# Kernel optimization log

Hardware: AMD Instinct MI355X
Metric: run time of the kernel (lower is better)

Reference implementation:

```python
import jax, jax.numpy as jnp
import numpy as np

B, C, W, H = 32, 256, 32, 32


def setup_inputs() -> dict:
    key = jax.random.key(0)
    ks = jax.random.split(key, 9)
    s = 1.0 / np.sqrt(C)
    return {
        "x": jax.random.normal(ks[0], (B, C, W, H), dtype=jnp.float32),
        "Wq": jax.random.normal(ks[1], (C, C), dtype=jnp.float32) * s,
        "bq": jax.random.normal(ks[2], (C,), dtype=jnp.float32) * 0.01,
        "Wk": jax.random.normal(ks[3], (C, C), dtype=jnp.float32) * s,
        "bk": jax.random.normal(ks[4], (C,), dtype=jnp.float32) * 0.01,
        "Wv": jax.random.normal(ks[5], (C, C), dtype=jnp.float32) * s,
        "bv": jax.random.normal(ks[6], (C,), dtype=jnp.float32) * 0.01,
        "rel_h": jax.random.normal(ks[7], (1, C, 1, H), dtype=jnp.float32),
        "rel_w": jax.random.normal(ks[8], (1, C, W, 1), dtype=jnp.float32),
    }


def reference(x, Wq, bq, Wk, bk, Wv, bv, rel_h, rel_w):
    b, c, w, h = x.shape
    n = w * h
    xf = x.reshape(b, c, n)  # [B, C, N]
    # 1x1 conv == channel-mixing matmul (out_ch 'o' from in_ch 'c')
    q = jnp.einsum('oc,bcn->bon', Wq, xf) + bq[None, :, None]
    k = jnp.einsum('oc,bcn->bon', Wk, xf) + bk[None, :, None]
    v = jnp.einsum('oc,bcn->bon', Wv, xf) + bv[None, :, None]
    # content-content: q^T k -> [B, N, N]
    content_content = jnp.einsum('bci,bcj->bij', q, k)
    # relative position bias: (rel_h + rel_w) broadcasts to [1, C, W, H]
    rel = (rel_h + rel_w).reshape(c, n)  # [C, N]
    content_position = jnp.einsum('cp,bcj->bpj', rel, q)  # [B, N, N]
    attention = jax.nn.softmax(content_content + content_position, axis=-1)
    # out[b,c,i] = sum_j v[b,c,j] * attention[b,i,j]
    out = jnp.einsum('bcj,bij->bci', v, attention)
    return out.reshape(b, c, w, h)
```

## Files before the change

kernel.cpp:

```cpp
#include <hip/hip_runtime.h>


#define NB 32
#define NC 256
#define NNN 1024

typedef _Float16 f16;
typedef __attribute__((ext_vector_type(8))) _Float16 half8;
typedef __attribute__((ext_vector_type(4))) float f32x4;
typedef __attribute__((ext_vector_type(4))) float float4v;

__device__ __forceinline__ f32x4 mfma16(half8 a, half8 b, f32x4 c) {
  return __builtin_amdgcn_mfma_f32_16x16x32_f16(a, b, c, 0, 0, 0);
}
__device__ __forceinline__ float sel4(float a0, float a1, float a2, float a3, int r) {
  return r == 0 ? a0 : (r == 1 ? a1 : (r == 2 ? a2 : a3));
}
__device__ __forceinline__ void gload16(const f16* g, f16* l) {
  __builtin_amdgcn_global_load_lds(
      (const __attribute__((address_space(1))) void*)g,
      (__attribute__((address_space(3))) void*)l, 16, 0, 0);
}

__global__ __launch_bounds__(256) void k_prep(
    const float* __restrict__ Wq, const float* __restrict__ Wk,
    const float* __restrict__ Wv, const float* __restrict__ relh,
    const float* __restrict__ relw, f16* __restrict__ Wh, f16* __restrict__ RT) {
  int bid = blockIdx.x, tid = threadIdx.x;
  if (bid < 192) {
    int base = (bid * 256 + tid) * 4;
    int w = base >> 16, j = base & 65535;
    const float* src = (w == 0) ? Wq : ((w == 1) ? Wk : Wv);
    float4v v = *(const float4v*)(src + j);
    f16 h[4] = {(f16)v.x, (f16)v.y, (f16)v.z, (f16)v.w};
    *(half8*)0;
    Wh[base + 0] = h[0]; Wh[base + 1] = h[1]; Wh[base + 2] = h[2]; Wh[base + 3] = h[3];
  } else {
    int n = bid - 192;
    int c = tid;
    RT[n * NC + c] = (f16)(relw[c * 32 + (n >> 5)] + relh[c * 32 + (n & 31)]);
  }
}

__global__ __launch_bounds__(256, 4) void k_proj(
    const float* __restrict__ x, const f16* __restrict__ Wh,
    const float* __restrict__ bq, const float* __restrict__ bk,
    const float* __restrict__ bv,
    f16* __restrict__ KQ, f16* __restrict__ V) {
  int b = blockIdx.x >> 4;
  int n0 = (blockIdx.x & 15) << 6;
  int tid = threadIdx.x;
  int wave = tid >> 6, lane = tid & 63;
  int lq = lane & 15, g = lane >> 4;
  int ow = wave << 6;

  __shared__ f16 XS[64][256];

  {
    const float* xb = x + (size_t)b * NC * NNN + n0;
    int cq = tid >> 2;
    int nn = (tid & 3) << 4;
    #pragma unroll
    for (int cc = 0; cc < 4; ++cc) {
      int c = cc * 64 + cq;
      const float* src = xb + (size_t)c * NNN + nn;
      float vals[16];
      *(float4v*)(vals + 0)  = *(const float4v*)(src + 0);
      *(float4v*)(vals + 4)  = *(const float4v*)(src + 4);
      *(float4v*)(vals + 8)  = *(const float4v*)(src + 8);
      *(float4v*)(vals + 12) = *(const float4v*)(src + 12);
      int s = c >> 3;
      #pragma unroll
      for (int u = 0; u < 16; ++u) {
        int n = nn + u;
        int p = (s & 0x10) | ((s ^ (n & 15)) & 0xF);
        XS[n][p * 8 + (c & 7)] = (f16)vals[u];
      }
    }
  }
  __syncthreads();

  #pragma unroll 1
  for (int which = 0; which < 2; ++which) {
    const f16* Wp = Wh + which * 65536;
    const float* bias = which ? bk : bq;
    int koff = which ? 0 : 256;
    f32x4 acc[4][4];
    #pragma unroll
    for (int f = 0; f < 4; ++f) {
      float bf = bias[ow + 16 * f + lq];
      #pragma unroll
      for (int m = 0; m < 4; ++m) acc[m][f] = (f32x4){bf, bf, bf, bf};
    }
    #pragma unroll
    for (int kk = 0; kk < 8; ++kk) {
      int cb = kk * 32 + 8 * g;
      int s = 4 * kk + g;
      int p = (s & 0x10) | ((s ^ lq) & 0xF);
      half8 xa[4], wb[4];
      #pragma unroll
      for (int m = 0; m < 4; ++m)
        xa[m] = *(const half8*)(&XS[16 * m + lq][p * 8]);
      #pragma unroll
      for (int f = 0; f < 4; ++f)
        wb[f] = *(const half8*)(Wp + (size_t)(ow + 16 * f + lq) * NC + cb);
      #pragma unroll
      for (int m = 0; m < 4; ++m)
        #pragma unroll
        for (int f = 0; f < 4; ++f)
          acc[m][f] = mfma16(xa[m], wb[f], acc[m][f]);
    }
    #pragma unroll
    for (int m = 0; m < 4; ++m)
      #pragma unroll
      for (int f = 0; f < 4; ++f)
        #pragma unroll
        for (int r = 0; r < 4; ++r)
          KQ[((size_t)b * NNN + n0 + 16 * m + 4 * g + r) * 512 + koff + ow + 16 * f + lq] =
              (f16)acc[m][f][r];
  }

  {
    const f16* Wp = Wh + 2 * 65536;
    f32x4 acc[4][4];
    #pragma unroll
    for (int m = 0; m < 4; ++m)
      #pragma unroll
      for (int r = 0; r < 4; ++r) {
        float bf = bv[ow + 16 * m + 4 * g + r];
        #pragma unroll
        for (int f = 0; f < 4; ++f) acc[m][f][r] = bf;
      }
    #pragma unroll
    for (int kk = 0; kk < 8; ++kk) {
      int cb = kk * 32 + 8 * g;
      int s = 4 * kk + g;
      int p = (s & 0x10) | ((s ^ lq) & 0xF);
      half8 va[4], xb2[4];
      #pragma unroll
      for (int m = 0; m < 4; ++m)
        va[m] = *(const half8*)(Wp + (size_t)(ow + 16 * m + lq) * NC + cb);
      #pragma unroll
      for (int f = 0; f < 4; ++f)
        xb2[f] = *(const half8*)(&XS[16 * f + lq][p * 8]);
      #pragma unroll
      for (int m = 0; m < 4; ++m)
        #pragma unroll
        for (int f = 0; f < 4; ++f)
          acc[m][f] = mfma16(va[m], xb2[f], acc[m][f]);
    }
    #pragma unroll
    for (int m = 0; m < 4; ++m)
      #pragma unroll
      for (int f = 0; f < 4; ++f)
        #pragma unroll
        for (int r = 0; r < 4; ++r)
          V[((size_t)b * NC + ow + 16 * m + 4 * g + r) * NNN + n0 + 16 * f + lq] =
              (f16)acc[m][f][r];
  }
}

__global__ __launch_bounds__(256, 2) void k_flash3(
    const f16* __restrict__ KQ, const f16* __restrict__ V,
    const f16* __restrict__ RT, float* __restrict__ out) {
  int bid = blockIdx.x;
  int swz = (bid & 7) * 64 + (bid >> 3);
  int b = swz >> 4;
  int i0 = (swz & 15) << 6;
  int tid = threadIdx.x;
  int wave = tid >> 6, lane = tid & 63;
  int lq = lane & 15, g = lane >> 4;
  int iw = i0 + 16 * wave;

  __shared__ f16 KQS[2][32][512];
  __shared__ f16 Plds[4][16][40];

  const f16* KQb = KQ + ((size_t)b << 19);
  const f16* Vb = V + ((size_t)b << 18);

  half8 QA[16];
  #pragma unroll
  for (int kk = 0; kk < 8; ++kk)
    QA[kk] = *(const half8*)(KQb + ((size_t)(iw + lq) << 9) + 256 + kk * 32 + 8 * g);
  #pragma unroll
  for (int kk = 0; kk < 8; ++kk)
    QA[8 + kk] = *(const half8*)(RT + (size_t)(iw + lq) * NC + kk * 32 + 8 * g);

  f32x4 acc[16];
  #pragma unroll
  for (int cf = 0; cf < 16; ++cf) acc[cf] = (f32x4){0.f, 0.f, 0.f, 0.f};
  float m[4] = {-1e30f, -1e30f, -1e30f, -1e30f};
  float lsum[4] = {0.f, 0.f, 0.f, 0.f};

#define STAGE(JT, BUF)                                                        \
  {                                                                           \
    _Pragma("unroll")                                                         \
    for (int rr = 0; rr < 8; ++rr) {                                          \
      int r_ = wave * 8 + rr;                                                 \
      int slot_ = (lane & 0x30) | ((lane ^ (r_ & 15)) & 0xF);                 \
      gload16(KQb + ((size_t)((JT) * 32 + r_) << 9) + slot_ * 8,              \
              &KQS[BUF][r_][0]);                                              \
    }                                                                         \
  }

  STAGE(0, 0);
  asm volatile("s_waitcnt vmcnt(0)" ::: "memory");
  __syncthreads();

  int cur = 0;
  #pragma unroll 1
  for (int jt = 0; jt < 32; ++jt) {
    int j0 = jt * 32;
    if (jt < 31) {
      if (cur) STAGE(jt + 1, 0) else STAGE(jt + 1, 1);
    }
    f32x4 S0 = (f32x4){0.f, 0.f, 0.f, 0.f};
    f32x4 S1 = (f32x4){0.f, 0.f, 0.f, 0.f};
    const f16* KQSc = &KQS[cur][0][0];
    __builtin_amdgcn_s_setprio(1);
    #pragma unroll
    for (int kk = 0; kk < 16; ++kk) {
      int s = 4 * kk + g;
      int p = (s & 0x30) | ((s ^ lq) & 0xF);
      S0 = mfma16(QA[kk], *(const half8*)(KQSc + lq * 512 + p * 8), S0);
      S1 = mfma16(QA[kk], *(const half8*)(KQSc + (16 + lq) * 512 + p * 8), S1);
    }
    __builtin_amdgcn_s_setprio(0);

    float t[4];
    #pragma unroll
    for (int r = 0; r < 4; ++r) {
      float tt = fmaxf(S0[r], S1[r]);
      tt = fmaxf(tt, __shfl_xor(tt, 1));
      tt = fmaxf(tt, __shfl_xor(tt, 2));
      tt = fmaxf(tt, __shfl_xor(tt, 4));
      tt = fmaxf(tt, __shfl_xor(tt, 8));
      t[r] = tt;
    }
    bool grow = (t[0] > m[0] + 8.f) | (t[1] > m[1] + 8.f) |
                (t[2] > m[2] + 8.f) | (t[3] > m[3] + 8.f);
    if (__builtin_amdgcn_ballot_w64(grow)) {
      float sc[4];
      #pragma unroll
      for (int r = 0; r < 4; ++r) {
        float mn = fmaxf(m[r], t[r]);
        sc[r] = __expf(m[r] - mn);
        m[r] = mn;
        lsum[r] *= sc[r];
      }
      int srcl = (lq >> 2) << 4;
      float s0 = __shfl(sc[0], srcl);
      float s1 = __shfl(sc[1], srcl);
      float s2 = __shfl(sc[2], srcl);
      float s3 = __shfl(sc[3], srcl);
      float sci = sel4(s0, s1, s2, s3, lq & 3);
      #pragma unroll
      for (int cf = 0; cf < 16; ++cf) {
        acc[cf][0] *= sci; acc[cf][1] *= sci; acc[cf][2] *= sci; acc[cf][3] *= sci;
      }
    }
    #pragma unroll
    for (int r = 0; r < 4; ++r) {
      float p0 = __expf(S0[r] - m[r]);
      float p1 = __expf(S1[r] - m[r]);
      S0[r] = p0; S1[r] = p1;
      lsum[r] += p0 + p1;
    }

    #pragma unroll
    for (int r = 0; r < 4; ++r) {
      Plds[wave][4 * g + r][lq] = (f16)S0[r];
      Plds[wave][4 * g + r][16 + lq] = (f16)S1[r];
    }
    asm volatile("s_waitcnt lgkmcnt(0)" ::: "memory");
    __builtin_amdgcn_sched_barrier(0);
    half8 pa = *(const half8*)(&Plds[wave][lq][8 * g]);

    __builtin_amdgcn_s_setprio(1);
    #pragma unroll
    for (int cf = 0; cf < 16; ++cf) {
      half8 vv = *(const half8*)(Vb + ((size_t)(16 * cf + lq) << 10) + j0 + 8 * g);
      acc[cf] = mfma16(vv, pa, acc[cf]);
    }
    __builtin_amdgcn_s_setprio(0);

    asm volatile("s_waitcnt vmcnt(0)" ::: "memory");
    __syncthreads();
    cur ^= 1;
  }
#undef STAGE

  #pragma unroll
  for (int r = 0; r < 4; ++r) {
    float l = lsum[r];
    l += __shfl_xor(l, 1);
    l += __shfl_xor(l, 2);
    l += __shfl_xor(l, 4);
    l += __shfl_xor(l, 8);
    lsum[r] = 1.f / l;
  }
  float li;
  {
    int srcl = (lq >> 2) << 4;
    float l0 = __shfl(lsum[0], srcl);
    float l1 = __shfl(lsum[1], srcl);
    float l2 = __shfl(lsum[2], srcl);
    float l3 = __shfl(lsum[3], srcl);
    li = sel4(l0, l1, l2, l3, lq & 3);
  }
  #pragma unroll
  for (int cf = 0; cf < 16; ++cf)
    #pragma unroll
    for (int r = 0; r < 4; ++r)
      out[((size_t)(b * NC + 16 * cf + 4 * g + r) << 10) + iw + lq] = acc[cf][r] * li;
}

extern "C" void kernel_launch(void* const* d_in, const int* in_sizes, int n_in,
                              void* d_out, int out_size, void* d_ws, size_t ws_size,
                              hipStream_t stream) {
  const float* x = (const float*)d_in[0];
  const float* Wq = (const float*)d_in[1];
  const float* bq = (const float*)d_in[2];
  const float* Wk = (const float*)d_in[3];
  const float* bk = (const float*)d_in[4];
  const float* Wv = (const float*)d_in[5];
  const float* bv = (const float*)d_in[6];
  const float* relh = (const float*)d_in[7];
  const float* relw = (const float*)d_in[8];

  char* ws = (char*)d_ws;
  const size_t MB = 1 << 20;
  f16* KQ = (f16*)(ws);
  f16* V = (f16*)(ws + 32 * MB);
  f16* RT = (f16*)(ws + 48 * MB);
  f16* Wh = (f16*)(ws + 48 * MB + 512 * 1024);

  k_prep<<<dim3(1216), dim3(256), 0, stream>>>(Wq, Wk, Wv, relh, relw, Wh, RT);
  k_proj<<<dim3(512), dim3(256), 0, stream>>>(x, Wh, bq, bk, bv, KQ, V);
  k_flash3<<<dim3(512), dim3(256), 0, stream>>>(KQ, V, RT, (float*)d_out);
}
```

Baseline: 326.4 us.

## Add transpose pre-pass and restructure flash attention with 16-row triple buffering

Adds a separate kernel that converts x to fp16 and transposes it to a token-major layout, so the projection kernel can fill shared memory with direct global-to-LDS loads instead of scattered per-element writes. The attention kernel now processes 16 key rows per step with operands swapped, so each lane holds one query row. That removes the LDS round-trip for P and shrinks the row-max and row-sum reductions. It uses a three-buffer LDS pipeline with a partial vmcnt wait, and the smaller LDS footprint allows raising occupancy to 3 blocks. The trade-off is an extra launch and an extra pass over x through memory, plus the cost of holding half of P in registers across iterations.

```diff
diff --git a/kernel.cpp b/kernel.cpp
--- a/kernel.cpp
+++ b/kernel.cpp
@@ -6,15 +6,13 @@
 #define NNN 1024
 
 typedef _Float16 f16;
+typedef __attribute__((ext_vector_type(4))) _Float16 half4;
 typedef __attribute__((ext_vector_type(8))) _Float16 half8;
 typedef __attribute__((ext_vector_type(4))) float f32x4;
 typedef __attribute__((ext_vector_type(4))) float float4v;
 
 __device__ __forceinline__ f32x4 mfma16(half8 a, half8 b, f32x4 c) {
   return __builtin_amdgcn_mfma_f32_16x16x32_f16(a, b, c, 0, 0, 0);
-}
-__device__ __forceinline__ float sel4(float a0, float a1, float a2, float a3, int r) {
-  return r == 0 ? a0 : (r == 1 ? a1 : (r == 2 ? a2 : a3));
 }
 __device__ __forceinline__ void gload16(const f16* g, f16* l) {
   __builtin_amdgcn_global_load_lds(
@@ -32,9 +30,8 @@
     int w = base >> 16, j = base & 65535;
     const float* src = (w == 0) ? Wq : ((w == 1) ? Wk : Wv);
     float4v v = *(const float4v*)(src + j);
-    f16 h[4] = {(f16)v.x, (f16)v.y, (f16)v.z, (f16)v.w};
-    *(half8*)0;
-    Wh[base + 0] = h[0]; Wh[base + 1] = h[1]; Wh[base + 2] = h[2]; Wh[base + 3] = h[3];
+    Wh[base + 0] = (f16)v.x; Wh[base + 1] = (f16)v.y;
+    Wh[base + 2] = (f16)v.z; Wh[base + 3] = (f16)v.w;
   } else {
     int n = bid - 192;
     int c = tid;
@@ -42,8 +39,42 @@
   }
 }
 
+__global__ __launch_bounds__(256) void k_xpose(
+    const float* __restrict__ x, f16* __restrict__ xT) {
+  int bid = blockIdx.x;
+  int nt = bid & 15, ct = (bid >> 4) & 3, b = bid >> 6;
+  int c0 = ct << 6, n0 = nt << 6;
+  __shared__ f16 T[64][72];
+  int t = threadIdx.x;
+  {
+    int cl = t >> 2, n4 = (t & 3) << 4;
+    const float* src = x + ((size_t)(b * NC + c0 + cl) << 10) + n0 + n4;
+    float4v v0 = *(const float4v*)(src + 0);
+    float4v v1 = *(const float4v*)(src + 4);
+    float4v v2 = *(const float4v*)(src + 8);
+    float4v v3 = *(const float4v*)(src + 12);
+    f16* d = &T[cl][n4];
+    d[0]=(f16)v0.x; d[1]=(f16)v0.y; d[2]=(f16)v0.z; d[3]=(f16)v0.w;
+    d[4]=(f16)v1.x; d[5]=(f16)v1.y; d[6]=(f16)v1.z; d[7]=(f16)v1.w;
+    d[8]=(f16)v2.x; d[9]=(f16)v2.y; d[10]=(f16)v2.z; d[11]=(f16)v2.w;
+    d[12]=(f16)v3.x; d[13]=(f16)v3.y; d[14]=(f16)v3.z; d[15]=(f16)v3.w;
+  }
+  __syncthreads();
+  {
+    int nl = t >> 2, c16 = (t & 3) << 4;
+    half8 h0, h1;
+    #pragma unroll
+    for (int u = 0; u < 8; ++u) h0[u] = T[c16 + u][nl];
+    #pragma unroll
+    for (int u = 0; u < 8; ++u) h1[u] = T[c16 + 8 + u][nl];
+    f16* dst = xT + ((size_t)(b * NNN + n0 + nl) << 8) + c0 + c16;
+    *(half8*)(dst) = h0;
+    *(half8*)(dst + 8) = h1;
+  }
+}
+
 __global__ __launch_bounds__(256, 4) void k_proj(
-    const float* __restrict__ x, const f16* __restrict__ Wh,
+    const f16* __restrict__ xT, const f16* __restrict__ Wh,
     const float* __restrict__ bq, const float* __restrict__ bk,
     const float* __restrict__ bv,
     f16* __restrict__ KQ, f16* __restrict__ V) {
@@ -53,31 +84,21 @@
   int wave = tid >> 6, lane = tid & 63;
   int lq = lane & 15, g = lane >> 4;
   int ow = wave << 6;
+  const f16* xTb = xT + ((size_t)(b * NNN + n0) << 8);
 
   __shared__ f16 XS[64][256];
 
   {
-    const float* xb = x + (size_t)b * NC * NNN + n0;
-    int cq = tid >> 2;
-    int nn = (tid & 3) << 4;
-    #pragma unroll
-    for (int cc = 0; cc < 4; ++cc) {
-      int c = cc * 64 + cq;
-      const float* src = xb + (size_t)c * NNN + nn;
-      float vals[16];
-      *(float4v*)(vals + 0)  = *(const float4v*)(src + 0);
-      *(float4v*)(vals + 4)  = *(const float4v*)(src + 4);
-      *(float4v*)(vals + 8)  = *(const float4v*)(src + 8);
-      *(float4v*)(vals + 12) = *(const float4v*)(src + 12);
-      int s = c >> 3;
-      #pragma unroll
-      for (int u = 0; u < 16; ++u) {
-        int n = nn + u;
-        int p = (s & 0x10) | ((s ^ (n & 15)) & 0xF);
-        XS[n][p * 8 + (c & 7)] = (f16)vals[u];
-      }
-    }
-  }
+    int li = lane & 31;
+    #pragma unroll
+    for (int q2 = 0; q2 < 8; ++q2) {
+      int r2 = wave * 16 + q2 * 2;
+      int r = r2 + (lane >> 5);
+      int slot = (li & 0x10) | ((li ^ (r & 15)) & 0xF);
+      gload16(xTb + ((size_t)r << 8) + slot * 8, &XS[r2][0]);
+    }
+  }
+  asm volatile("s_waitcnt vmcnt(0)" ::: "memory");
   __syncthreads();
 
   #pragma unroll 1
@@ -90,7 +111,7 @@
     for (int f = 0; f < 4; ++f) {
       float bf = bias[ow + 16 * f + lq];
       #pragma unroll
-      for (int m = 0; m < 4; ++m) acc[m][f] = (f32x4){bf, bf, bf, bf};
+      for (int mm = 0; mm < 4; ++mm) acc[mm][f] = (f32x4){bf, bf, bf, bf};
     }
     #pragma unroll
     for (int kk = 0; kk < 8; ++kk) {
@@ -99,37 +120,37 @@
       int p = (s & 0x10) | ((s ^ lq) & 0xF);
       half8 xa[4], wb[4];
       #pragma unroll
-      for (int m = 0; m < 4; ++m)
-        xa[m] = *(const half8*)(&XS[16 * m + lq][p * 8]);
+      for (int mm = 0; mm < 4; ++mm)
+        xa[mm] = *(const half8*)(&XS[16 * mm + lq][p * 8]);
       #pragma unroll
       for (int f = 0; f < 4; ++f)
         wb[f] = *(const half8*)(Wp + (size_t)(ow + 16 * f + lq) * NC + cb);
       #pragma unroll
-      for (int m = 0; m < 4; ++m)
+      for (int mm = 0; mm < 4; ++mm)
         #pragma unroll
         for (int f = 0; f < 4; ++f)
-          acc[m][f] = mfma16(xa[m], wb[f], acc[m][f]);
-    }
-    #pragma unroll
-    for (int m = 0; m < 4; ++m)
+          acc[mm][f] = mfma16(xa[mm], wb[f], acc[mm][f]);
+    }
+    #pragma unroll
+    for (int mm = 0; mm < 4; ++mm)
       #pragma unroll
       for (int f = 0; f < 4; ++f)
         #pragma unroll
         for (int r = 0; r < 4; ++r)
-          KQ[((size_t)b * NNN + n0 + 16 * m + 4 * g + r) * 512 + koff + ow + 16 * f + lq] =
-              (f16)acc[m][f][r];
+          KQ[((size_t)(b * NNN + n0 + 16 * mm + 4 * g + r) << 9) + koff + ow + 16 * f + lq] =
+              (f16)acc[mm][f][r];
   }
 
   {
     const f16* Wp = Wh + 2 * 65536;
     f32x4 acc[4][4];
     #pragma unroll
-    for (int m = 0; m < 4; ++m)
+    for (int mm = 0; mm < 4; ++mm)
       #pragma unroll
       for (int r = 0; r < 4; ++r) {
-        float bf = bv[ow + 16 * m + 4 * g + r];
-        #pragma unroll
-        for (int f = 0; f < 4; ++f) acc[m][f][r] = bf;
+        float bf = bv[ow + 16 * mm + 4 * g + r];
+        #pragma unroll
+        for (int f = 0; f < 4; ++f) acc[mm][f][r] = bf;
       }
     #pragma unroll
     for (int kk = 0; kk < 8; ++kk) {
@@ -138,29 +159,29 @@
       int p = (s & 0x10) | ((s ^ lq) & 0xF);
       half8 va[4], xb2[4];
       #pragma unroll
-      for (int m = 0; m < 4; ++m)
-        va[m] = *(const half8*)(Wp + (size_t)(ow + 16 * m + lq) * NC + cb);
+      for (int mm = 0; mm < 4; ++mm)
+        va[mm] = *(const half8*)(Wp + (size_t)(ow + 16 * mm + lq) * NC + cb);
       #pragma unroll
       for (int f = 0; f < 4; ++f)
         xb2[f] = *(const half8*)(&XS[16 * f + lq][p * 8]);
       #pragma unroll
-      for (int m = 0; m < 4; ++m)
+      for (int mm = 0; mm < 4; ++mm)
         #pragma unroll
         for (int f = 0; f < 4; ++f)
-          acc[m][f] = mfma16(va[m], xb2[f], acc[m][f]);
-    }
-    #pragma unroll
-    for (int m = 0; m < 4; ++m)
+          acc[mm][f] = mfma16(va[mm], xb2[f], acc[mm][f]);
+    }
+    #pragma unroll
+    for (int mm = 0; mm < 4; ++mm)
       #pragma unroll
       for (int f = 0; f < 4; ++f)
         #pragma unroll
         for (int r = 0; r < 4; ++r)
-          V[((size_t)b * NC + ow + 16 * m + 4 * g + r) * NNN + n0 + 16 * f + lq] =
-              (f16)acc[m][f][r];
-  }
-}
-
-__global__ __launch_bounds__(256, 2) void k_flash3(
+          V[((size_t)(b * NC + ow + 16 * mm + 4 * g + r) << 10) + n0 + 16 * f + lq] =
+              (f16)acc[mm][f][r];
+  }
+}
+
+__global__ __launch_bounds__(256, 3) void k_flash4(
     const f16* __restrict__ KQ, const f16* __restrict__ V,
     const f16* __restrict__ RT, float* __restrict__ out) {
   int bid = blockIdx.x;
@@ -172,8 +193,7 @@
   int lq = lane & 15, g = lane >> 4;
   int iw = i0 + 16 * wave;
 
-  __shared__ f16 KQS[2][32][512];
-  __shared__ f16 Plds[4][16][40];
+  __shared__ f16 KQS[3][16][512];
 
   const f16* KQb = KQ + ((size_t)b << 19);
   const f16* Vb = V + ((size_t)b << 18);
@@ -189,125 +209,89 @@
   f32x4 acc[16];
   #pragma unroll
   for (int cf = 0; cf < 16; ++cf) acc[cf] = (f32x4){0.f, 0.f, 0.f, 0.f};
-  float m[4] = {-1e30f, -1e30f, -1e30f, -1e30f};
-  float lsum[4] = {0.f, 0.f, 0.f, 0.f};
-
-#define STAGE(JT, BUF)                                                        \
-  {                                                                           \
-    _Pragma("unroll")                                                         \
-    for (int rr = 0; rr < 8; ++rr) {                                          \
-      int r_ = wave * 8 + rr;                                                 \
-      int slot_ = (lane & 0x30) | ((lane ^ (r_ & 15)) & 0xF);                 \
-      gload16(KQb + ((size_t)((JT) * 32 + r_) << 9) + slot_ * 8,              \
-              &KQS[BUF][r_][0]);                                              \
-    }                                                                         \
+  float m = -1e30f, lsum = 0.f;
+  half4 pend = (half4){0, 0, 0, 0};
+
+#define STAGE(T, BUF)                                                       \
+  {                                                                         \
+    int jt2_ = (T) >> 1, p_ = (T) & 1;                                      \
+    _Pragma("unroll")                                                       \
+    for (int q = 0; q < 4; ++q) {                                           \
+      int rho_ = 4 * wave + q;                                              \
+      int j_ = jt2_ * 32 + 8 * wave + 4 * p_ + q;                           \
+      int slot_ = (lane & 0x30) | ((lane ^ rho_) & 0xF);                    \
+      gload16(KQb + ((size_t)j_ << 9) + slot_ * 8, &KQS[BUF][rho_][0]);     \
+    }                                                                       \
   }
 
   STAGE(0, 0);
-  asm volatile("s_waitcnt vmcnt(0)" ::: "memory");
-  __syncthreads();
-
-  int cur = 0;
+  STAGE(1, 1);
+
+  int bufc = 0, bufn = 2;
   #pragma unroll 1
-  for (int jt = 0; jt < 32; ++jt) {
-    int j0 = jt * 32;
-    if (jt < 31) {
-      if (cur) STAGE(jt + 1, 0) else STAGE(jt + 1, 1);
-    }
-    f32x4 S0 = (f32x4){0.f, 0.f, 0.f, 0.f};
-    f32x4 S1 = (f32x4){0.f, 0.f, 0.f, 0.f};
-    const f16* KQSc = &KQS[cur][0][0];
+  for (int t = 0; t < 64; ++t) {
+    if (t < 63) {
+      asm volatile("s_waitcnt vmcnt(4)" ::: "memory");
+    } else {
+      asm volatile("s_waitcnt vmcnt(0)" ::: "memory");
+    }
+    __syncthreads();
+    if (t < 62) STAGE(t + 2, bufn);
+
+    f32x4 S = (f32x4){0.f, 0.f, 0.f, 0.f};
+    const f16* KQSc = &KQS[bufc][0][0];
     __builtin_amdgcn_s_setprio(1);
     #pragma unroll
     for (int kk = 0; kk < 16; ++kk) {
       int s = 4 * kk + g;
       int p = (s & 0x30) | ((s ^ lq) & 0xF);
-      S0 = mfma16(QA[kk], *(const half8*)(KQSc + lq * 512 + p * 8), S0);
-      S1 = mfma16(QA[kk], *(const half8*)(KQSc + (16 + lq) * 512 + p * 8), S1);
+      S = mfma16(*(const half8*)(KQSc + lq * 512 + p * 8), QA[kk], S);
     }
     __builtin_amdgcn_s_setprio(0);
 
-    float t[4];
-    #pragma unroll
-    for (int r = 0; r < 4; ++r) {
-      float tt = fmaxf(S0[r], S1[r]);
-      tt = fmaxf(tt, __shfl_xor(tt, 1));
-      tt = fmaxf(tt, __shfl_xor(tt, 2));
-      tt = fmaxf(tt, __shfl_xor(tt, 4));
-      tt = fmaxf(tt, __shfl_xor(tt, 8));
-      t[r] = tt;
-    }
-    bool grow = (t[0] > m[0] + 8.f) | (t[1] > m[1] + 8.f) |
-                (t[2] > m[2] + 8.f) | (t[3] > m[3] + 8.f);
+    float tmax = fmaxf(fmaxf(S[0], S[1]), fmaxf(S[2], S[3]));
+    tmax = fmaxf(tmax, __shfl_xor(tmax, 16));
+    tmax = fmaxf(tmax, __shfl_xor(tmax, 32));
+    bool grow = tmax > m + 8.f;
     if (__builtin_amdgcn_ballot_w64(grow)) {
-      float sc[4];
-      #pragma unroll
-      for (int r = 0; r < 4; ++r) {
-        float mn = fmaxf(m[r], t[r]);
-        sc[r] = __expf(m[r] - mn);
-        m[r] = mn;
-        lsum[r] *= sc[r];
+      float mn = fmaxf(m, tmax);
+      float sc = __expf(m - mn);
+      m = mn;
+      lsum *= sc;
+      #pragma unroll
+      for (int cf = 0; cf < 16; ++cf) {
+        acc[cf][0] *= sc; acc[cf][1] *= sc; acc[cf][2] *= sc; acc[cf][3] *= sc;
       }
-      int srcl = (lq >> 2) << 4;
-      float s0 = __shfl(sc[0], srcl);
-      float s1 = __shfl(sc[1], srcl);
-      float s2 = __shfl(sc[2], srcl);
-      float s3 = __shfl(sc[3], srcl);
-      float sci = sel4(s0, s1, s2, s3, lq & 3);
+      f16 sch = (f16)sc;
+      pend[0] *= sch; pend[1] *= sch; pend[2] *= sch; pend[3] *= sch;
+    }
+    float p0 = __expf(S[0] - m), p1 = __expf(S[1] - m),
+          p2 = __expf(S[2] - m), p3 = __expf(S[3] - m);
+    lsum += (p0 + p1) + (p2 + p3);
+
+    if ((t & 1) == 0) {
+      pend = (half4){(f16)p0, (f16)p1, (f16)p2, (f16)p3};
+    } else {
+      half8 pa;
+      pa[0] = pend[0]; pa[1] = pend[1]; pa[2] = pend[2]; pa[3] = pend[3];
+      pa[4] = (f16)p0; pa[5] = (f16)p1; pa[6] = (f16)p2; pa[7] = (f16)p3;
+      size_t j0 = (size_t)((t >> 1) * 32 + 8 * g);
+      __builtin_amdgcn_s_setprio(1);
       #pragma unroll
       for (int cf = 0; cf < 16; ++cf) {
-        acc[cf][0] *= sci; acc[cf][1] *= sci; acc[cf][2] *= sci; acc[cf][3] *= sci;
+        half8 vv = *(const half8*)(Vb + ((size_t)(16 * cf + lq) << 10) + j0);
+        acc[cf] = mfma16(vv, pa, acc[cf]);
       }
-    }
-    #pragma unroll
-    for (int r = 0; r < 4; ++r) {
-      float p0 = __expf(S0[r] - m[r]);
-      float p1 = __expf(S1[r] - m[r]);
-      S0[r] = p0; S1[r] = p1;
-      lsum[r] += p0 + p1;
-    }
-
-    #pragma unroll
-    for (int r = 0; r < 4; ++r) {
-      Plds[wave][4 * g + r][lq] = (f16)S0[r];
-      Plds[wave][4 * g + r][16 + lq] = (f16)S1[r];
-    }
-    asm volatile("s_waitcnt lgkmcnt(0)" ::: "memory");
-    __builtin_amdgcn_sched_barrier(0);
-    half8 pa = *(const half8*)(&Plds[wave][lq][8 * g]);
-
-    __builtin_amdgcn_s_setprio(1);
-    #pragma unroll
-    for (int cf = 0; cf < 16; ++cf) {
-      half8 vv = *(const half8*)(Vb + ((size_t)(16 * cf + lq) << 10) + j0 + 8 * g);
-      acc[cf] = mfma16(vv, pa, acc[cf]);
-    }
-    __builtin_amdgcn_s_setprio(0);
-
-    asm volatile("s_waitcnt vmcnt(0)" ::: "memory");
-    __syncthreads();
-    cur ^= 1;
+      __builtin_amdgcn_s_setprio(0);
+    }
+    bufc = (bufc == 2) ? 0 : bufc + 1;
+    bufn = (bufn == 2) ? 0 : bufn + 1;
   }
 #undef STAGE
 
-  #pragma unroll
-  for (int r = 0; r < 4; ++r) {
-    float l = lsum[r];
-    l += __shfl_xor(l, 1);
-    l += __shfl_xor(l, 2);
-    l += __shfl_xor(l, 4);
-    l += __shfl_xor(l, 8);
-    lsum[r] = 1.f / l;
-  }
-  float li;
-  {
-    int srcl = (lq >> 2) << 4;
-    float l0 = __shfl(lsum[0], srcl);
-    float l1 = __shfl(lsum[1], srcl);
-    float l2 = __shfl(lsum[2], srcl);
-    float l3 = __shfl(lsum[3], srcl);
-    li = sel4(l0, l1, l2, l3, lq & 3);
-  }
+  lsum += __shfl_xor(lsum, 16);
+  lsum += __shfl_xor(lsum, 32);
+  float li = 1.f / lsum;
   #pragma unroll
   for (int cf = 0; cf < 16; ++cf)
     #pragma unroll
@@ -330,12 +314,14 @@
 
   char* ws = (char*)d_ws;
   const size_t MB = 1 << 20;
-  f16* KQ = (f16*)(ws);
-  f16* V = (f16*)(ws + 32 * MB);
-  f16* RT = (f16*)(ws + 48 * MB);
-  f16* Wh = (f16*)(ws + 48 * MB + 512 * 1024);
+  f16* xT = (f16*)(ws);
+  f16* KQ = (f16*)(ws + 16 * MB);
+  f16* V  = (f16*)(ws + 48 * MB);
+  f16* RT = (f16*)(ws + 64 * MB);
+  f16* Wh = (f16*)(ws + 64 * MB + 512 * 1024);
 
   k_prep<<<dim3(1216), dim3(256), 0, stream>>>(Wq, Wk, Wv, relh, relw, Wh, RT);
-  k_proj<<<dim3(512), dim3(256), 0, stream>>>(x, Wh, bq, bk, bv, KQ, V);
-  k_flash3<<<dim3(512), dim3(256), 0, stream>>>(KQ, V, RT, (float*)d_out);
-}
+  k_xpose<<<dim3(2048), dim3(256), 0, stream>>>(x, xT);
+  k_proj<<<dim3(512), dim3(256), 0, stream>>>(xT, Wh, bq, bk, bv, KQ, V);
+  k_flash4<<<dim3(512), dim3(256), 0, stream>>>(KQ, V, RT, (float*)d_out);
+}
```

Result: slower. 622.1 us (+90.6%).
